# Performance work log

Measured on AMD Instinct MI355X. Metric: run time of the kernel, lower is better.

## Reference

```python
import jax, jax.numpy as jnp
import numpy as np

B, T, OBS = 256, 512, 256
H = 128          # OptimizedLSTMCell hidden size (hardcoded in module)
LATENT = 16


def setup_inputs() -> dict:
    key = jax.random.key(0)
    ks = jax.random.split(key, 6)
    xs = jax.random.normal(ks[0], (B, T, OBS), dtype=jnp.float32)
    # fused LSTM weights: gates ordered (i, f, g, o), each of width H
    Wx = jax.random.normal(ks[1], (OBS, 4 * H), dtype=jnp.float32) / np.sqrt(OBS)
    Wh = jax.random.normal(ks[2], (H, 4 * H), dtype=jnp.float32) / np.sqrt(H)
    b = jnp.zeros((4 * H,), dtype=jnp.float32)
    W1 = jax.random.normal(ks[3], (H, H), dtype=jnp.float32) / np.sqrt(H)
    b1 = jnp.zeros((H,), dtype=jnp.float32)
    W2 = jax.random.normal(ks[4], (H, 2 * LATENT), dtype=jnp.float32) / np.sqrt(H)
    b2 = jnp.zeros((2 * LATENT,), dtype=jnp.float32)
    return {"xs": xs, "Wx": Wx, "Wh": Wh, "b": b,
            "W1": W1, "b1": b1, "W2": W2, "b2": b2}


def reference(xs, Wx, Wh, b, W1, b1, W2, b2):
    # LSTM over time (flax OptimizedLSTMCell math, zero initial carry)
    bsz = xs.shape[0]
    hdim = Wh.shape[0]

    def step(carry, x_t):
        c, h = carry
        gates = x_t @ Wx + h @ Wh + b            # [B, 4H]
        i, f, g, o = jnp.split(gates, 4, axis=-1)
        i = jax.nn.sigmoid(i)
        f = jax.nn.sigmoid(f)
        g = jnp.tanh(g)
        o = jax.nn.sigmoid(o)
        c = f * c + i * g
        h = o * jnp.tanh(c)
        return (c, h), None

    init = (jnp.zeros((bsz, hdim), xs.dtype), jnp.zeros((bsz, hdim), xs.dtype))
    (_, h_last), _ = jax.lax.scan(step, init, jnp.swapaxes(xs, 0, 1))

    out = jax.nn.relu(h_last @ W1 + b1)          # [B, H]
    p = out @ W2 + b2                            # [B, 2*latent]
    mean, logvar = jnp.split(p, 2, axis=-1)
    return mean, logvar
```

## Files before the change

kernel.cpp:

```cpp
#include <hip/hip_runtime.h>
#include <hip/hip_fp16.h>

typedef unsigned short u16;
typedef unsigned int u32;

#define B_   256
#define T_   512
#define OBS_ 256
#define H_   128
#define G4_  512
#define LAT_ 16

typedef _Float16 half8_t __attribute__((ext_vector_type(8)));
typedef _Float16 half2_t __attribute__((ext_vector_type(2)));
typedef float    f32x4_t __attribute__((ext_vector_type(4)));

#if defined(__has_builtin)
#if __has_builtin(__builtin_amdgcn_fdot2)
#define HAVE_FDOT2 1
#endif
#endif

__device__ __forceinline__ u16 f2h(float x) { return __half_as_ushort(__float2half(x)); }
__device__ __forceinline__ float h2f(u16 u) { return __half2float(__ushort_as_half(u)); }
__device__ __forceinline__ float frcp(float x) { return __builtin_amdgcn_rcpf(x); }
__device__ __forceinline__ float fsigmoid(float x) { return frcp(1.f + __expf(-x)); }
__device__ __forceinline__ float ftanh(float x) { return 1.f - 2.f * frcp(1.f + __expf(2.f * x)); }

__device__ __forceinline__ float dot2acc(u32 w, u32 h, float acc) {
  half2_t wv = __builtin_bit_cast(half2_t, w);
  half2_t hv = __builtin_bit_cast(half2_t, h);
#ifdef HAVE_FDOT2
  return __builtin_amdgcn_fdot2(wv, hv, acc, false);
#else
  acc = fmaf((float)wv.x, (float)wv.x, acc);
  acc = fmaf((float)wv.y, (float)hv.y, acc);
  return acc;
#endif
}

__device__ __forceinline__ float quad_sum(float x) {
  int xi = __builtin_bit_cast(int, x);
  int y1 = __builtin_amdgcn_update_dpp(xi, xi, 0xB1, 0xF, 0xF, false);
  float s1 = x + __builtin_bit_cast(float, y1);
  int si = __builtin_bit_cast(int, s1);
  int y2 = __builtin_amdgcn_update_dpp(si, si, 0x4E, 0xF, 0xF, false);
  return s1 + __builtin_bit_cast(float, y2);
}

__device__ __forceinline__ int permcol(int n) { return (n & 3) * 128 + (n >> 2); }

__global__ __launch_bounds__(256) void prep_kernel(const float* __restrict__ Wx,
                                                   const float* __restrict__ Wh,
                                                   const float* __restrict__ bias,
                                                   u16* __restrict__ Wxt,
                                                   u32* __restrict__ Whp,
                                                   float* __restrict__ biasp) {
  int idx = blockIdx.x * 256 + threadIdx.x;
  if (idx < G4_ * OBS_) {
    int n = idx / OBS_, k = idx % OBS_;
    Wxt[idx] = f2h(Wx[(size_t)k * G4_ + permcol(n)]);
  } else if (idx < G4_ * OBS_ + (H_ / 2) * G4_) {
    int i2 = idx - G4_ * OBS_;
    int k2 = i2 / G4_, n = i2 % G4_;
    int pn = permcol(n);
    u32 lo = f2h(Wh[(size_t)(2 * k2) * G4_ + pn]);
    u32 hi = f2h(Wh[(size_t)(2 * k2 + 1) * G4_ + pn]);
    Whp[i2] = lo | (hi << 16);
  } else if (idx < G4_ * OBS_ + (H_ / 2) * G4_ + G4_) {
    int n = idx - G4_ * OBS_ - (H_ / 2) * G4_;
    biasp[n] = bias[permcol(n)];
  }
}

__global__ __launch_bounds__(256, 2) void gemm_xw(const float* __restrict__ xs,
                                                  const u16* __restrict__ Wxt,
                                                  u16* __restrict__ Xw,
                                                  int t0, int ct_log2) {
  __shared__ __align__(16) u16 As[128][88];
  __shared__ __align__(16) u16 Bs[128][88];

  const int tid  = threadIdx.x;
  const int lane = tid & 63;
  const int w    = tid >> 6;
  const int qr   = (w & 1) * 64;
  const int qc   = (w >> 1) * 64;
  const int bn   = blockIdx.x;
  const int bm   = blockIdx.y;

  f32x4_t acc[4][4];
#pragma unroll
  for (int a = 0; a < 4; ++a)
#pragma unroll
    for (int bq = 0; bq < 4; ++bq)
      acc[a][bq] = (f32x4_t){0.f, 0.f, 0.f, 0.f};

  const int row  = tid >> 1;
  const int half = (tid & 1) * 32;
  const int m    = bm * 128 + row;
  const int bb   = m >> ct_log2;
  const int tau  = m & ((1 << ct_log2) - 1);
  const float* asrc = xs + (size_t)(bb * T_ + t0 + tau) * OBS_ + half;
  const u16*   bsrc = Wxt + (size_t)(bn * 128 + row) * OBS_ + half;

  for (int k0 = 0; k0 < OBS_; k0 += 64) {
    {
      const float* s = asrc + k0;
#pragma unroll
      for (int i = 0; i < 4; ++i) {
        float4 v0 = *(const float4*)(s + i * 8);
        float4 v1 = *(const float4*)(s + i * 8 + 4);
        uint4 pk;
        pk.x = (u32)f2h(v0.x) | ((u32)f2h(v0.y) << 16);
        pk.y = (u32)f2h(v0.z) | ((u32)f2h(v0.w) << 16);
        pk.z = (u32)f2h(v1.x) | ((u32)f2h(v1.y) << 16);
        pk.w = (u32)f2h(v1.z) | ((u32)f2h(v1.w) << 16);
        *(uint4*)&As[row][half + i * 8] = pk;
      }
    }
    {
      const u16* s = bsrc + k0;
#pragma unroll
      for (int i = 0; i < 4; ++i)
        *(uint4*)&Bs[row][half + i * 8] = *(const uint4*)(s + i * 8);
    }
    __syncthreads();
#pragma unroll
    for (int ks = 0; ks < 2; ++ks) {
      const int kc = ks * 32 + (lane >> 4) * 8;
      half8_t af[4], bf[4];
#pragma unroll
      for (int mi = 0; mi < 4; ++mi) af[mi] = *(const half8_t*)&As[qr + mi * 16 + (lane & 15)][kc];
#pragma unroll
      for (int ni = 0; ni < 4; ++ni) bf[ni] = *(const half8_t*)&Bs[qc + ni * 16 + (lane & 15)][kc];
#pragma unroll
      for (int mi = 0; mi < 4; ++mi)
#pragma unroll
        for (int ni = 0; ni < 4; ++ni)
          acc[mi][ni] = __builtin_amdgcn_mfma_f32_16x16x32_f16(af[mi], bf[ni], acc[mi][ni], 0, 0, 0);
    }
    __syncthreads();
  }
#pragma unroll
  for (int mi = 0; mi < 4; ++mi)
#pragma unroll
    for (int ni = 0; ni < 4; ++ni)
#pragma unroll
      for (int r = 0; r < 4; ++r) {
        int mm = bm * 128 + qr + mi * 16 + (lane >> 4) * 4 + r;
        int nn = bn * 128 + qc + ni * 16 + (lane & 15);
        Xw[(size_t)mm * G4_ + nn] = f2h(acc[mi][ni][r]);
      }
}

__global__ __launch_bounds__(512) __attribute__((amdgpu_waves_per_eu(2, 2)))
void lstm_rec(const u16* __restrict__ Xw,
              const u32* __restrict__ Whp,
              const float* __restrict__ biasp,
              float* __restrict__ c_ws,
              u16* __restrict__ h_ws,
              int t0, int CT) {
  const int bb  = blockIdx.x;
  const int tid = threadIdx.x;
  const int s   = tid & 3;
  const int j   = tid >> 2;
  __shared__ u32 hq[2][64];

  uint4 W[16];
  {
    const u32* base = Whp + (size_t)(16 * s) * 512 + 4 * j;
#pragma unroll
    for (int r = 0; r < 16; ++r)
      asm volatile("global_load_dwordx4 %0, %1, off"
                   : "=v"(W[r]) : "v"(base + (size_t)r * 512));
  }
  const float4 bj = *(const float4*)(biasp + 4 * j);

  const u16* xwrow = Xw + (size_t)bb * CT * 512 + 4 * j;
  uint2 x0, x1, x2, x3;
  asm volatile("global_load_dwordx2 %0, %1, off"             : "=v"(x0) : "v"(xwrow));
  asm volatile("global_load_dwordx2 %0, %1, off offset:1024" : "=v"(x1) : "v"(xwrow));
  asm volatile("global_load_dwordx2 %0, %1, off offset:2048" : "=v"(x2) : "v"(xwrow));
  asm volatile("global_load_dwordx2 %0, %1, off offset:3072" : "=v"(x3) : "v"(xwrow));

  float c = 0.f;
  if (t0 == 0) {
    if (tid < 64) hq[0][tid] = 0u;
  } else {
    if (tid < 64) hq[0][tid] = ((const u32*)h_ws)[bb * 64 + tid];
    c = c_ws[bb * 128 + j];
  }
  asm volatile("s_waitcnt vmcnt(0)" ::: "memory");
  __builtin_amdgcn_sched_barrier(0);
  __syncthreads();

  float hval = 0.f;

  auto step = [&](uint2 xw, int cur) {
    const u32* hp = &hq[cur][16 * s];
    uint4 h0 = *(const uint4*)(hp);
    uint4 h1 = *(const uint4*)(hp + 4);
    uint4 h2 = *(const uint4*)(hp + 8);
    uint4 h3 = *(const uint4*)(hp + 12);
    u32 hv[16] = {h0.x, h0.y, h0.z, h0.w, h1.x, h1.y, h1.z, h1.w,
                  h2.x, h2.y, h2.z, h2.w, h3.x, h3.y, h3.z, h3.w};

    float p0 = 0.f, p1 = 0.f, p2 = 0.f, p3 = 0.f;
#pragma unroll
    for (int r = 0; r < 16; ++r) {
      p0 = dot2acc(W[r].x, hv[r], p0);
      p1 = dot2acc(W[r].y, hv[r], p1);
      p2 = dot2acc(W[r].z, hv[r], p2);
      p3 = dot2acc(W[r].w, hv[r], p3);
    }
    p0 = quad_sum(p0);
    p1 = quad_sum(p1);
    p2 = quad_sum(p2);
    p3 = quad_sum(p3);

    half2_t xlo = __builtin_bit_cast(half2_t, xw.x);
    half2_t xhi = __builtin_bit_cast(half2_t, xw.y);
    float ig = fsigmoid(p0 + bj.x + (float)xlo.x);
    float fg = fsigmoid(p1 + bj.y + (float)xlo.y);
    float gg = ftanh   (p2 + bj.z + (float)xhi.x);
    float og = fsigmoid(p3 + bj.w + (float)xhi.y);
    c = fg * c + ig * gg;
    hval = og * ftanh(c);
    if (s == 0) ((u16*)&hq[cur ^ 1][0])[j] = f2h(hval);
    __syncthreads();
  };

  int t = 0;
  for (; t < CT - 4; t += 4) {
    uint2 n0, n1, n2, n3;
    const u16* p4 = xwrow + (size_t)(t + 4) * 512;
    asm volatile("global_load_dwordx2 %0, %1, off"             : "=v"(n0) : "v"(p4));
    asm volatile("global_load_dwordx2 %0, %1, off offset:1024" : "=v"(n1) : "v"(p4));
    asm volatile("global_load_dwordx2 %0, %1, off offset:2048" : "=v"(n2) : "v"(p4));
    asm volatile("global_load_dwordx2 %0, %1, off offset:3072" : "=v"(n3) : "v"(p4));
    asm volatile("s_waitcnt vmcnt(4)" ::: "memory");
    __builtin_amdgcn_sched_barrier(0);
    step(x0, 0);
    step(x1, 1);
    step(x2, 0);
    step(x3, 1);
    x0 = n0; x1 = n1; x2 = n2; x3 = n3;
  }
  asm volatile("s_waitcnt vmcnt(0)" ::: "memory");
  __builtin_amdgcn_sched_barrier(0);
  step(x0, 0);
  step(x1, 1);
  step(x2, 0);
  step(x3, 1);

  if (s == 0) {
    c_ws[bb * 128 + j] = c;
    h_ws[bb * 128 + j] = f2h(hval);
  }
}

__global__ __launch_bounds__(128) void head_kernel(const u16* __restrict__ h_ws,
                                                   const float* __restrict__ W1,
                                                   const float* __restrict__ b1,
                                                   const float* __restrict__ W2,
                                                   const float* __restrict__ b2,
                                                   float* __restrict__ out) {
  const int bb = blockIdx.x;
  const int j  = threadIdx.x;
  __shared__ float hs[128];
  __shared__ float o1[128];
  hs[j] = h2f(h_ws[bb * 128 + j]);
  __syncthreads();
  float acc = b1[j];
#pragma unroll 8
  for (int k = 0; k < 128; ++k) acc = fmaf(hs[k], W1[(size_t)k * 128 + j], acc);
  o1[j] = fmaxf(acc, 0.f);
  __syncthreads();
  if (j < 2 * LAT_) {
    float acc2 = b2[j];
#pragma unroll 8
    for (int k = 0; k < 128; ++k) acc2 = fmaf(o1[k], W2[(size_t)k * (2 * LAT_) + j], acc2);
    if (j < LAT_) out[(size_t)bb * LAT_ + j] = acc2;
    else          out[(size_t)B_ * LAT_ + (size_t)bb * LAT_ + (j - LAT_)] = acc2;
  }
}

extern "C" void kernel_launch(void* const* d_in, const int* in_sizes, int n_in,
                              void* d_out, int out_size, void* d_ws, size_t ws_size,
                              hipStream_t stream) {
  const float* xs   = (const float*)d_in[0];
  const float* Wx   = (const float*)d_in[1];
  const float* Wh   = (const float*)d_in[2];
  const float* bias = (const float*)d_in[3];
  const float* W1   = (const float*)d_in[4];
  const float* b1   = (const float*)d_in[5];
  const float* W2   = (const float*)d_in[6];
  const float* b2   = (const float*)d_in[7];
  float* out = (float*)d_out;

  char* ws = (char*)d_ws;
  u16* Wxt    = (u16*)(ws + 0);
  u32* Whp    = (u32*)(ws + 262144);
  float* c_ws = (float*)(ws + 393216);
  u16* h_ws   = (u16*)(ws + 524288);
  float* biasp= (float*)(ws + 589824);
  u16* Xw     = (u16*)(ws + 591872);

  int CT = 512;
  while (CT > 128 && 591872 + (size_t)262144 * CT > ws_size) CT >>= 1;
  int ctl = __builtin_ctz((unsigned)CT);

  prep_kernel<<<642, 256, 0, stream>>>(Wx, Wh, bias, Wxt, Whp, biasp);
  for (int t0 = 0; t0 < T_; t0 += CT) {
    gemm_xw<<<dim3(4, 2 * CT), 256, 0, stream>>>(xs, Wxt, Xw, t0, ctl);
    lstm_rec<<<256, 512, 0, stream>>>(Xw, Whp, biasp, c_ws, h_ws, t0, CT);
  }
  head_kernel<<<256, 128, 0, stream>>>(h_ws, W1, b1, W2, b2, out);
}
```

Measured before the change: 475.4 us.

## Pack two batch rows per 1024-thread block in LSTM recurrence

```diff
diff --git a/kernel.cpp b/kernel.cpp
--- a/kernel.cpp
+++ b/kernel.cpp
@@ -33,7 +33,7 @@
 #ifdef HAVE_FDOT2
   return __builtin_amdgcn_fdot2(wv, hv, acc, false);
 #else
-  acc = fmaf((float)wv.x, (float)wv.x, acc);
+  acc = fmaf((float)wv.x, (float)hv.x, acc);
   acc = fmaf((float)wv.y, (float)hv.y, acc);
   return acc;
 #endif
@@ -105,11 +105,11 @@
 
   for (int k0 = 0; k0 < OBS_; k0 += 64) {
     {
-      const float* s = asrc + k0;
+      const float* sp = asrc + k0;
 #pragma unroll
       for (int i = 0; i < 4; ++i) {
-        float4 v0 = *(const float4*)(s + i * 8);
-        float4 v1 = *(const float4*)(s + i * 8 + 4);
+        float4 v0 = *(const float4*)(sp + i * 8);
+        float4 v1 = *(const float4*)(sp + i * 8 + 4);
         uint4 pk;
         pk.x = (u32)f2h(v0.x) | ((u32)f2h(v0.y) << 16);
         pk.y = (u32)f2h(v0.z) | ((u32)f2h(v0.w) << 16);
@@ -119,10 +119,10 @@
       }
     }
     {
-      const u16* s = bsrc + k0;
+      const u16* sp = bsrc + k0;
 #pragma unroll
       for (int i = 0; i < 4; ++i)
-        *(uint4*)&Bs[row][half + i * 8] = *(const uint4*)(s + i * 8);
+        *(uint4*)&Bs[row][half + i * 8] = *(const uint4*)(sp + i * 8);
     }
     __syncthreads();
 #pragma unroll
@@ -153,18 +153,20 @@
       }
 }
 
-__global__ __launch_bounds__(512) __attribute__((amdgpu_waves_per_eu(2, 2)))
+__global__ __launch_bounds__(1024) __attribute__((amdgpu_waves_per_eu(4, 4)))
 void lstm_rec(const u16* __restrict__ Xw,
               const u32* __restrict__ Whp,
               const float* __restrict__ biasp,
               float* __restrict__ c_ws,
               u16* __restrict__ h_ws,
               int t0, int CT) {
-  const int bb  = blockIdx.x;
-  const int tid = threadIdx.x;
-  const int s   = tid & 3;
-  const int j   = tid >> 2;
-  __shared__ u32 hq[2][64];
+  const int tid  = threadIdx.x;
+  const int half = tid >> 9;
+  const int tloc = tid & 511;
+  const int bb   = blockIdx.x * 2 + half;
+  const int s    = tloc & 3;
+  const int j    = tloc >> 2;
+  __shared__ u32 hq[2][2][64];
 
   uint4 W[16];
   {
@@ -185,9 +187,9 @@
 
   float c = 0.f;
   if (t0 == 0) {
-    if (tid < 64) hq[0][tid] = 0u;
+    if (tloc < 64) hq[half][0][tloc] = 0u;
   } else {
-    if (tid < 64) hq[0][tid] = ((const u32*)h_ws)[bb * 64 + tid];
+    if (tloc < 64) hq[half][0][tloc] = ((const u32*)h_ws)[bb * 64 + tloc];
     c = c_ws[bb * 128 + j];
   }
   asm volatile("s_waitcnt vmcnt(0)" ::: "memory");
@@ -197,22 +199,46 @@
   float hval = 0.f;
 
   auto step = [&](uint2 xw, int cur) {
-    const u32* hp = &hq[cur][16 * s];
+    const u32* hp = &hq[half][cur][16 * s];
     uint4 h0 = *(const uint4*)(hp);
     uint4 h1 = *(const uint4*)(hp + 4);
     uint4 h2 = *(const uint4*)(hp + 8);
     uint4 h3 = *(const uint4*)(hp + 12);
-    u32 hv[16] = {h0.x, h0.y, h0.z, h0.w, h1.x, h1.y, h1.z, h1.w,
-                  h2.x, h2.y, h2.z, h2.w, h3.x, h3.y, h3.z, h3.w};
 
     float p0 = 0.f, p1 = 0.f, p2 = 0.f, p3 = 0.f;
-#pragma unroll
-    for (int r = 0; r < 16; ++r) {
-      p0 = dot2acc(W[r].x, hv[r], p0);
-      p1 = dot2acc(W[r].y, hv[r], p1);
-      p2 = dot2acc(W[r].z, hv[r], p2);
-      p3 = dot2acc(W[r].w, hv[r], p3);
-    }
+    p0 = dot2acc(W[0].x, h0.x, p0);  p1 = dot2acc(W[0].y, h0.x, p1);
+    p2 = dot2acc(W[0].z, h0.x, p2);  p3 = dot2acc(W[0].w, h0.x, p3);
+    p0 = dot2acc(W[1].x, h0.y, p0);  p1 = dot2acc(W[1].y, h0.y, p1);
+    p2 = dot2acc(W[1].z, h0.y, p2);  p3 = dot2acc(W[1].w, h0.y, p3);
+    p0 = dot2acc(W[2].x, h0.z, p0);  p1 = dot2acc(W[2].y, h0.z, p1);
+    p2 = dot2acc(W[2].z, h0.z, p2);  p3 = dot2acc(W[2].w, h0.z, p3);
+    p0 = dot2acc(W[3].x, h0.w, p0);  p1 = dot2acc(W[3].y, h0.w, p1);
+    p2 = dot2acc(W[3].z, h0.w, p2);  p3 = dot2acc(W[3].w, h0.w, p3);
+    p0 = dot2acc(W[4].x, h1.x, p0);  p1 = dot2acc(W[4].y, h1.x, p1);
+    p2 = dot2acc(W[4].z, h1.x, p2);  p3 = dot2acc(W[4].w, h1.x, p3);
+    p0 = dot2acc(W[5].x, h1.y, p0);  p1 = dot2acc(W[5].y, h1.y, p1);
+    p2 = dot2acc(W[5].z, h1.y, p2);  p3 = dot2acc(W[5].w, h1.y, p3);
+    p0 = dot2acc(W[6].x, h1.z, p0);  p1 = dot2acc(W[6].y, h1.z, p1);
+    p2 = dot2acc(W[6].z, h1.z, p2);  p3 = dot2acc(W[6].w, h1.z, p3);
+    p0 = dot2acc(W[7].x, h1.w, p0);  p1 = dot2acc(W[7].y, h1.w, p1);
+    p2 = dot2acc(W[7].z, h1.w, p2);  p3 = dot2acc(W[7].w, h1.w, p3);
+    p0 = dot2acc(W[8].x, h2.x, p0);  p1 = dot2acc(W[8].y, h2.x, p1);
+    p2 = dot2acc(W[8].z, h2.x, p2);  p3 = dot2acc(W[8].w, h2.x, p3);
+    p0 = dot2acc(W[9].x, h2.y, p0);  p1 = dot2acc(W[9].y, h2.y, p1);
+    p2 = dot2acc(W[9].z, h2.y, p2);  p3 = dot2acc(W[9].w, h2.y, p3);
+    p0 = dot2acc(W[10].x, h2.z, p0); p1 = dot2acc(W[10].y, h2.z, p1);
+    p2 = dot2acc(W[10].z, h2.z, p2); p3 = dot2acc(W[10].w, h2.z, p3);
+    p0 = dot2acc(W[11].x, h2.w, p0); p1 = dot2acc(W[11].y, h2.w, p1);
+    p2 = dot2acc(W[11].z, h2.w, p2); p3 = dot2acc(W[11].w, h2.w, p3);
+    p0 = dot2acc(W[12].x, h3.x, p0); p1 = dot2acc(W[12].y, h3.x, p1);
+    p2 = dot2acc(W[12].z, h3.x, p2); p3 = dot2acc(W[12].w, h3.x, p3);
+    p0 = dot2acc(W[13].x, h3.y, p0); p1 = dot2acc(W[13].y, h3.y, p1);
+    p2 = dot2acc(W[13].z, h3.y, p2); p3 = dot2acc(W[13].w, h3.y, p3);
+    p0 = dot2acc(W[14].x, h3.z, p0); p1 = dot2acc(W[14].y, h3.z, p1);
+    p2 = dot2acc(W[14].z, h3.z, p2); p3 = dot2acc(W[14].w, h3.z, p3);
+    p0 = dot2acc(W[15].x, h3.w, p0); p1 = dot2acc(W[15].y, h3.w, p1);
+    p2 = dot2acc(W[15].z, h3.w, p2); p3 = dot2acc(W[15].w, h3.w, p3);
+
     p0 = quad_sum(p0);
     p1 = quad_sum(p1);
     p2 = quad_sum(p2);
@@ -226,7 +252,7 @@
     float og = fsigmoid(p3 + bj.w + (float)xhi.y);
     c = fg * c + ig * gg;
     hval = og * ftanh(c);
-    if (s == 0) ((u16*)&hq[cur ^ 1][0])[j] = f2h(hval);
+    if (s == 0) ((u16*)&hq[half][cur ^ 1][0])[j] = f2h(hval);
     __syncthreads();
   };
 
@@ -313,7 +339,7 @@
   prep_kernel<<<642, 256, 0, stream>>>(Wx, Wh, bias, Wxt, Whp, biasp);
   for (int t0 = 0; t0 < T_; t0 += CT) {
     gemm_xw<<<dim3(4, 2 * CT), 256, 0, stream>>>(xs, Wxt, Xw, t0, ctl);
-    lstm_rec<<<256, 512, 0, stream>>>(Xw, Whp, biasp, c_ws, h_ws, t0, CT);
+    lstm_rec<<<128, 1024, 0, stream>>>(Xw, Whp, biasp, c_ws, h_ws, t0, CT);
   }
   head_kernel<<<256, 128, 0, stream>>>(h_ws, W1, b1, W2, b2, out);
 }
```

After: 705.4 us. 1.48x slower.
